# Optimization experiments

Measured on AMD Instinct MI355X. Metric: run time of the kernel, lower is better.

Reference implementation:

```python
import jax, jax.numpy as jnp
import numpy as np

B, L, D, K = 8, 1024, 1024, 128
VOCAB, N_ATOM_FEAT, N_TIMESTEPS = 160, 512, 1000
NEG = jnp.finfo(jnp.float32).min
SCALING = K ** (-0.5)


def setup_inputs() -> dict:
    key = jax.random.key(0)
    ks = jax.random.split(key, 14)
    inp = {}
    # forward args
    inp["token_id"] = jax.random.randint(ks[0], (B, L), 0, VOCAB)  # 0 => padding
    inp["node_attr"] = jax.random.randint(ks[1], (B, L, 9), 0, N_ATOM_FEAT)
    inp["is_molecule"] = jax.random.randint(ks[2], (B,), 0, 2).astype(bool)
    inp["pos"] = jax.random.normal(ks[3], (B, L, 3), jnp.float32) * 10.0
    inp["time_step"] = jax.random.randint(ks[4], (B, L), 0, N_TIMESTEPS)
    # learned parameters
    inp["embed_table"] = jax.random.normal(ks[5], (VOCAB, D), jnp.float32) * 0.02
    inp["atom_feat_table"] = jax.random.normal(ks[6], (N_ATOM_FEAT, D), jnp.float32) * 0.02
    inp["time_table"] = jax.random.normal(ks[7], (N_TIMESTEPS, D), jnp.float32) * 0.02
    inp["time_w1"] = jax.random.normal(ks[8], (D, D), jnp.float32) * (D ** -0.5)
    inp["time_b1"] = jnp.zeros((D,), jnp.float32)
    inp["time_w2"] = jax.random.normal(ks[9], (D, D), jnp.float32) * (D ** -0.5)
    inp["time_b2"] = jnp.zeros((D,), jnp.float32)
    inp["pos_emb_w"] = jax.random.normal(ks[10], (1, K), jnp.float32)          # Linear(1 -> K), no bias
    inp["pos_feature_w"] = jax.random.normal(ks[11], (K, D), jnp.float32) * (K ** -0.5)  # Linear(K -> D), no bias
    return inp


def _pos_emb(pos, padding_mask, pos_emb_w, pos_feature_w):
    # pos: [B,L,3], padding_mask: [B,L] bool
    delta = pos[:, :, None, :] - pos[:, None, :, :]          # [B,L,L,3]
    dist = 1.0 / (jnp.linalg.norm(delta, axis=-1) + 1.0)     # [B,L,L]
    # masked_fill on key side (expand_mask) and query side (padding_mask)
    mask = padding_mask[:, None, :] | padding_mask[:, :, None]
    dist = jnp.where(mask, NEG, dist)
    # value projection: Linear(1->K) on per-atom radial norm, zeroed at padding
    pe = jnp.linalg.norm(pos, axis=-1, keepdims=True) @ pos_emb_w  # [B,L,K]
    pe = jnp.where(padding_mask[:, :, None], 0.0, pe)
    attn = jax.nn.softmax(dist * SCALING, axis=-1)            # [B,L,L]
    pfe = jnp.einsum("bqk,bkc->bqc", attn, pe)                 # [B,L,K]
    pfe = pfe @ pos_feature_w                                  # [B,L,D]
    return jnp.where(padding_mask[:, :, None], 0.0, pfe)


def reference(token_id, node_attr, is_molecule, pos, time_step,
              embed_table, atom_feat_table, time_table,
              time_w1, time_b1, time_w2, time_b2,
              pos_emb_w, pos_feature_w):
    padding_mask = token_id == 0                               # [B,L]
    x = embed_table[token_id]                                  # [B,L,D]
    # 2D atom features: embed cols 1: and sum over feature axis
    atom_emb = atom_feat_table[node_attr[:, :, 1:]].sum(axis=-2)  # [B,L,D]
    atom_emb = jnp.where(is_molecule[:, None, None], atom_emb, 0.0)
    x = x + atom_emb
    # time step encoder: learnable embedding + Linear-SiLU-Linear MLP
    t = time_table[time_step]                                   # [B,L,D]
    time_embed = jax.nn.silu(t @ time_w1 + time_b1) @ time_w2 + time_b2
    x = x + time_embed
    # pairwise 3D positional embedding (softmax attention over 1/(r+1))
    x = x + _pos_emb(pos, padding_mask, pos_emb_w, pos_feature_w)
    return x, padding_mask
```

## Files before the change

kernel.cpp:

```cpp
#include <hip/hip_runtime.h>
#include <hip/hip_bf16.h>
#include <math.h>

#define BB 8
#define LL 1024
#define DD 1024
#define KK 128
#define NTS 1000
#define NEGF -3.40282346638528859811704183485e38f
#define SCALE 0.08838834764831845f

typedef __attribute__((ext_vector_type(8))) short short8;
typedef __attribute__((ext_vector_type(4))) float f32x4;

__device__ __forceinline__ unsigned short f2bf(float x) {
    __hip_bfloat16 h = __float2bfloat16(x);
    return *reinterpret_cast<unsigned short*>(&h);
}

__global__ __launch_bounds__(256) void setup_kernel(
    const float* __restrict__ pos,
    const float* __restrict__ pos_emb_w,
    const float* __restrict__ pos_feature_w,
    const void*  __restrict__ is_mol_raw,
    float* __restrict__ norms,
    float* __restrict__ v,
    int*   __restrict__ is_mol_out)
{
    int gb = blockIdx.x;
    if (gb < 32) {
        int i = gb * 256 + threadIdx.x;
        float x = pos[i * 3 + 0];
        float y = pos[i * 3 + 1];
        float z = pos[i * 3 + 2];
        norms[i] = sqrtf(x * x + y * y + z * z);
    } else if (gb < 36) {
        int d = (gb - 32) * 256 + threadIdx.x;
        float acc = 0.0f;
        #pragma unroll 4
        for (int c = 0; c < KK; ++c)
            acc += pos_emb_w[c] * pos_feature_w[c * DD + d];
        v[d] = acc;
    } else {
        if (threadIdx.x == 0) {
            const int* ip = (const int*)is_mol_raw;
            const unsigned char* cp = (const unsigned char*)is_mol_raw;
            bool all_bin = true;
            for (int i = 0; i < BB; ++i) {
                int x = ip[i];
                if (x != 0 && x != 1) all_bin = false;
            }
            for (int i = 0; i < BB; ++i)
                is_mol_out[i] = all_bin ? (ip[i] != 0) : (cp[i] != 0);
        }
    }
}

__global__ __launch_bounds__(256) void cast_pad_kernel(
    const float* __restrict__ in, unsigned short* __restrict__ out)
{
    int i = blockIdx.x * 256 + threadIdx.x;
    int e = i * 4;
    ushort4 o;
    if (e < NTS * DD) {
        float4 vv = *(const float4*)&in[e];
        o.x = f2bf(vv.x); o.y = f2bf(vv.y); o.z = f2bf(vv.z); o.w = f2bf(vv.w);
    } else {
        o.x = o.y = o.z = o.w = 0;
    }
    *(ushort4*)&out[e] = o;
}

__global__ __launch_bounds__(256) void transpose_cast_kernel(
    const float* __restrict__ in, unsigned short* __restrict__ out)
{
    __shared__ float tile[32][33];
    const int tx = threadIdx.x & 31, ty = threadIdx.x >> 5;
    const int bx = blockIdx.x * 32, by = blockIdx.y * 32;
    #pragma unroll
    for (int r = 0; r < 32; r += 8)
        tile[ty + r][tx] = in[(size_t)(by + ty + r) * DD + bx + tx];
    __syncthreads();
    #pragma unroll
    for (int r = 0; r < 32; r += 8)
        out[(size_t)(bx + ty + r) * DD + by + tx] = f2bf(tile[tx][ty + r]);
}

template <int MODE>
__global__ __launch_bounds__(256) void mfma_gemm(
    const unsigned short* __restrict__ A,
    const unsigned short* __restrict__ Bt,
    const float* __restrict__ bias,
    void* __restrict__ Cout)
{
    __shared__ __align__(16) unsigned short As[64][72];
    __shared__ __align__(16) unsigned short Bs[64][72];

    const int tid  = threadIdx.x;
    const int lane = tid & 63;
    const int wave = tid >> 6;
    const int wm = wave >> 1, wn = wave & 1;
    const int quad = lane >> 4, l16 = lane & 15;
    const int mBase = blockIdx.y * 64, nBase = blockIdx.x * 64;

    f32x4 acc[2][2] = {{{0.f,0.f,0.f,0.f},{0.f,0.f,0.f,0.f}},
                       {{0.f,0.f,0.f,0.f},{0.f,0.f,0.f,0.f}}};

    const int r0 = tid >> 3,           ko0 = (tid & 7) << 3;
    const int r1 = (tid + 256) >> 3,   ko1 = ko0;

    for (int k0 = 0; k0 < DD; k0 += 64) {
        float4 a0 = *(const float4*)&A [(size_t)(mBase + r0) * DD + k0 + ko0];
        float4 a1 = *(const float4*)&A [(size_t)(mBase + r1) * DD + k0 + ko1];
        float4 b0 = *(const float4*)&Bt[(size_t)(nBase + r0) * DD + k0 + ko0];
        float4 b1 = *(const float4*)&Bt[(size_t)(nBase + r1) * DD + k0 + ko1];
        *(float4*)&As[r0][ko0] = a0;
        *(float4*)&As[r1][ko1] = a1;
        *(float4*)&Bs[r0][ko0] = b0;
        *(float4*)&Bs[r1][ko1] = b1;
        __syncthreads();

        #pragma unroll
        for (int kk = 0; kk < 64; kk += 32) {
            short8 af0 = *(const short8*)&As[wm * 32 +      l16][kk + quad * 8];
            short8 af1 = *(const short8*)&As[wm * 32 + 16 + l16][kk + quad * 8];
            short8 bf0 = *(const short8*)&Bs[wn * 32 +      l16][kk + quad * 8];
            short8 bf1 = *(const short8*)&Bs[wn * 32 + 16 + l16][kk + quad * 8];
            acc[0][0] = __builtin_amdgcn_mfma_f32_16x16x32_bf16(af0, bf0, acc[0][0], 0, 0, 0);
            acc[0][1] = __builtin_amdgcn_mfma_f32_16x16x32_bf16(af0, bf1, acc[0][1], 0, 0, 0);
            acc[1][0] = __builtin_amdgcn_mfma_f32_16x16x32_bf16(af1, bf0, acc[1][0], 0, 0, 0);
            acc[1][1] = __builtin_amdgcn_mfma_f32_16x16x32_bf16(af1, bf1, acc[1][1], 0, 0, 0);
        }
        __syncthreads();
    }

    #pragma unroll
    for (int mi = 0; mi < 2; ++mi) {
        #pragma unroll
        for (int ni = 0; ni < 2; ++ni) {
            const int col = nBase + wn * 32 + ni * 16 + l16;
            const float bv = bias[col];
            #pragma unroll
            for (int r = 0; r < 4; ++r) {
                const int row = mBase + wm * 32 + mi * 16 + quad * 4 + r;
                float val = acc[mi][ni][r] + bv;
                if (MODE == 0) {
                    val = val / (1.0f + expf(-val));
                    ((unsigned short*)Cout)[(size_t)row * DD + col] = f2bf(val);
                } else {
                    ((float*)Cout)[(size_t)row * DD + col] = val;
                }
            }
        }
    }
}

__global__ __launch_bounds__(256) void fused_out(
    const int*   __restrict__ token_id,
    const int*   __restrict__ node_attr,
    const float* __restrict__ pos,
    const int*   __restrict__ time_step,
    const float* __restrict__ embed_table,
    const float* __restrict__ atom_feat_table,
    const float* __restrict__ E,
    const float* __restrict__ v,
    const float* __restrict__ norms,
    const int*   __restrict__ is_mol,
    float* __restrict__ out)
{
    __shared__ float redA[256];
    __shared__ float redB[256];

    const int t   = blockIdx.x;
    const int b   = t >> 10;
    const int tid = threadIdx.x;

    const int token = token_id[t];
    const bool padq = (token == 0);

    const float qx = pos[t * 3 + 0];
    const float qy = pos[t * 3 + 1];
    const float qz = pos[t * 3 + 2];

    float dv[4], wv[4];
    float lmax = -INFINITY;
    #pragma unroll
    for (int i = 0; i < 4; ++i) {
        int k = tid + i * 256;
        int kt = token_id[b * LL + k];
        float kx = pos[(b * LL + k) * 3 + 0];
        float ky = pos[(b * LL + k) * 3 + 1];
        float kz = pos[(b * LL + k) * 3 + 2];
        float dx = qx - kx, dy = qy - ky, dz = qz - kz;
        float dn = sqrtf(dx * dx + dy * dy + dz * dz);
        float dist = (padq || kt == 0) ? NEGF : 1.0f / (dn + 1.0f);
        float dsc = dist * SCALE;
        dv[i] = dsc;
        wv[i] = (kt == 0) ? 0.0f : norms[b * LL + k];
        lmax = fmaxf(lmax, dsc);
    }
    redA[tid] = lmax;
    __syncthreads();
    for (int off = 128; off > 0; off >>= 1) {
        if (tid < off) redA[tid] = fmaxf(redA[tid], redA[tid + off]);
        __syncthreads();
    }
    const float gmax = redA[0];
    __syncthreads();

    float lsum = 0.0f, lws = 0.0f;
    #pragma unroll
    for (int i = 0; i < 4; ++i) {
        float e = expf(dv[i] - gmax);
        lsum += e;
        lws  += e * wv[i];
    }
    redA[tid] = lsum;
    redB[tid] = lws;
    __syncthreads();
    for (int off = 128; off > 0; off >>= 1) {
        if (tid < off) {
            redA[tid] += redA[tid + off];
            redB[tid] += redB[tid + off];
        }
        __syncthreads();
    }
    const float s = redB[0] / redA[0];

    const int ts = time_step[t];
    const int j = tid * 4;

    float4 acc = *(const float4*)&embed_table[(size_t)token * DD + j];
    if (is_mol[b]) {
        #pragma unroll
        for (int f = 1; f < 9; ++f) {
            int a = node_attr[t * 9 + f];
            float4 av = *(const float4*)&atom_feat_table[(size_t)a * DD + j];
            acc.x += av.x; acc.y += av.y; acc.z += av.z; acc.w += av.w;
        }
    }
    float4 ev = *(const float4*)&E[(size_t)ts * DD + j];
    acc.x += ev.x; acc.y += ev.y; acc.z += ev.z; acc.w += ev.w;

    if (!padq) {
        float4 vv = *(const float4*)&v[j];
        acc.x += s * vv.x; acc.y += s * vv.y; acc.z += s * vv.z; acc.w += s * vv.w;
    }
    *(float4*)&out[(size_t)t * DD + j] = acc;

    if (tid == 0)
        out[(size_t)BB * LL * DD + t] = padq ? 1.0f : 0.0f;
}

extern "C" void kernel_launch(void* const* d_in, const int* in_sizes, int n_in,
                              void* d_out, int out_size, void* d_ws, size_t ws_size,
                              hipStream_t stream)
{
    const int*   token_id      = (const int*)  d_in[0];
    const int*   node_attr     = (const int*)  d_in[1];
    const void*  is_mol_raw    = (const void*) d_in[2];
    const float* pos           = (const float*)d_in[3];
    const int*   time_step     = (const int*)  d_in[4];
    const float* embed_table   = (const float*)d_in[5];
    const float* atom_feat     = (const float*)d_in[6];
    const float* time_table    = (const float*)d_in[7];
    const float* w1            = (const float*)d_in[8];
    const float* b1            = (const float*)d_in[9];
    const float* w2            = (const float*)d_in[10];
    const float* b2            = (const float*)d_in[11];
    const float* pos_emb_w     = (const float*)d_in[12];
    const float* pos_feature_w = (const float*)d_in[13];

    float* out = (float*)d_out;
    float* Wf  = (float*)d_ws;

    unsigned short* Tbf = (unsigned short*)Wf;
    unsigned short* W1t = (unsigned short*)(Wf + 524288);
    float*          E   = Wf;
    unsigned short* H   = (unsigned short*)(Wf + 1048576);
    unsigned short* W2t = (unsigned short*)(Wf + 1048576 + 524288);
    float* V     = Wf + 2097152;
    float* norms = V + 1024;
    int*   is_mol_res = (int*)(norms + BB * LL);

    setup_kernel<<<37, 256, 0, stream>>>(pos, pos_emb_w, pos_feature_w,
                                         is_mol_raw, norms, V, is_mol_res);
    cast_pad_kernel<<<1024, 256, 0, stream>>>(time_table, Tbf);
    transpose_cast_kernel<<<dim3(32, 32), 256, 0, stream>>>(w1, W1t);
    transpose_cast_kernel<<<dim3(32, 32), 256, 0, stream>>>(w2, W2t);

    dim3 g(16, 16);
    mfma_gemm<0><<<g, 256, 0, stream>>>(Tbf, W1t, b1, (void*)H);
    mfma_gemm<1><<<g, 256, 0, stream>>>(H, W2t, b2, (void*)E);

    fused_out<<<8192, 256, 0, stream>>>(token_id, node_attr, pos, time_step,
                                        embed_table, atom_feat, E, V, norms,
                                        is_mol_res, out);
}
```

Before: 173.1 us.

## Merge prep kernels and restructure softmax to eight queries per block

```diff
diff --git a/kernel.cpp b/kernel.cpp
--- a/kernel.cpp
+++ b/kernel.cpp
@@ -7,7 +7,6 @@
 #define DD 1024
 #define KK 128
 #define NTS 1000
-#define NEGF -3.40282346638528859811704183485e38f
 #define SCALE 0.08838834764831845f
 
 typedef __attribute__((ext_vector_type(8))) short short8;
@@ -18,24 +17,48 @@
     return *reinterpret_cast<unsigned short*>(&h);
 }
 
-__global__ __launch_bounds__(256) void setup_kernel(
-    const float* __restrict__ pos,
+__global__ __launch_bounds__(256) void prep_kernel(
+    const float* __restrict__ time_table,
+    const float* __restrict__ w1,
+    const float* __restrict__ w2,
     const float* __restrict__ pos_emb_w,
     const float* __restrict__ pos_feature_w,
     const void*  __restrict__ is_mol_raw,
-    float* __restrict__ norms,
+    unsigned short* __restrict__ Tbf,
+    unsigned short* __restrict__ W1t,
+    unsigned short* __restrict__ W2t,
     float* __restrict__ v,
     int*   __restrict__ is_mol_out)
 {
-    int gb = blockIdx.x;
-    if (gb < 32) {
-        int i = gb * 256 + threadIdx.x;
-        float x = pos[i * 3 + 0];
-        float y = pos[i * 3 + 1];
-        float z = pos[i * 3 + 2];
-        norms[i] = sqrtf(x * x + y * y + z * z);
-    } else if (gb < 36) {
-        int d = (gb - 32) * 256 + threadIdx.x;
+    __shared__ float tile[32][33];
+    const int blk = blockIdx.x;
+
+    if (blk < 1024) {
+        int e = (blk * 256 + threadIdx.x) * 4;
+        ushort4 o;
+        if (e < NTS * DD) {
+            float4 vv = *(const float4*)&time_table[e];
+            o.x = f2bf(vv.x); o.y = f2bf(vv.y); o.z = f2bf(vv.z); o.w = f2bf(vv.w);
+        } else {
+            o.x = o.y = o.z = o.w = 0;
+        }
+        *(ushort4*)&Tbf[e] = o;
+    } else if (blk < 3072) {
+        const int which = (blk - 1024) >> 10;
+        const int idx = (blk - 1024) & 1023;
+        const float* in = which ? w2 : w1;
+        unsigned short* out = which ? W2t : W1t;
+        const int bx = (idx & 31) * 32, by = (idx >> 5) * 32;
+        const int tx = threadIdx.x & 31, ty = threadIdx.x >> 5;
+        #pragma unroll
+        for (int r = 0; r < 32; r += 8)
+            tile[ty + r][tx] = in[(size_t)(by + ty + r) * DD + bx + tx];
+        __syncthreads();
+        #pragma unroll
+        for (int r = 0; r < 32; r += 8)
+            out[(size_t)(bx + ty + r) * DD + by + tx] = f2bf(tile[tx][ty + r]);
+    } else if (blk < 3076) {
+        int d = (blk - 3072) * 256 + threadIdx.x;
         float acc = 0.0f;
         #pragma unroll 4
         for (int c = 0; c < KK; ++c)
@@ -56,36 +79,6 @@
     }
 }
 
-__global__ __launch_bounds__(256) void cast_pad_kernel(
-    const float* __restrict__ in, unsigned short* __restrict__ out)
-{
-    int i = blockIdx.x * 256 + threadIdx.x;
-    int e = i * 4;
-    ushort4 o;
-    if (e < NTS * DD) {
-        float4 vv = *(const float4*)&in[e];
-        o.x = f2bf(vv.x); o.y = f2bf(vv.y); o.z = f2bf(vv.z); o.w = f2bf(vv.w);
-    } else {
-        o.x = o.y = o.z = o.w = 0;
-    }
-    *(ushort4*)&out[e] = o;
-}
-
-__global__ __launch_bounds__(256) void transpose_cast_kernel(
-    const float* __restrict__ in, unsigned short* __restrict__ out)
-{
-    __shared__ float tile[32][33];
-    const int tx = threadIdx.x & 31, ty = threadIdx.x >> 5;
-    const int bx = blockIdx.x * 32, by = blockIdx.y * 32;
-    #pragma unroll
-    for (int r = 0; r < 32; r += 8)
-        tile[ty + r][tx] = in[(size_t)(by + ty + r) * DD + bx + tx];
-    __syncthreads();
-    #pragma unroll
-    for (int r = 0; r < 32; r += 8)
-        out[(size_t)(bx + ty + r) * DD + by + tx] = f2bf(tile[tx][ty + r]);
-}
-
 template <int MODE>
 __global__ __launch_bounds__(256) void mfma_gemm(
     const unsigned short* __restrict__ A,
@@ -106,8 +99,8 @@
     f32x4 acc[2][2] = {{{0.f,0.f,0.f,0.f},{0.f,0.f,0.f,0.f}},
                        {{0.f,0.f,0.f,0.f},{0.f,0.f,0.f,0.f}}};
 
-    const int r0 = tid >> 3,           ko0 = (tid & 7) << 3;
-    const int r1 = (tid + 256) >> 3,   ko1 = ko0;
+    const int r0 = tid >> 3,         ko0 = (tid & 7) << 3;
+    const int r1 = (tid + 256) >> 3, ko1 = ko0;
 
     for (int k0 = 0; k0 < DD; k0 += 64) {
         float4 a0 = *(const float4*)&A [(size_t)(mBase + r0) * DD + k0 + ko0];
@@ -155,7 +148,7 @@
     }
 }
 
-__global__ __launch_bounds__(256) void fused_out(
+__global__ __launch_bounds__(256) void fused_all(
     const int*   __restrict__ token_id,
     const int*   __restrict__ node_attr,
     const float* __restrict__ pos,
@@ -164,92 +157,88 @@
     const float* __restrict__ atom_feat_table,
     const float* __restrict__ E,
     const float* __restrict__ v,
-    const float* __restrict__ norms,
     const int*   __restrict__ is_mol,
     float* __restrict__ out)
 {
-    __shared__ float redA[256];
-    __shared__ float redB[256];
-
-    const int t   = blockIdx.x;
-    const int b   = t >> 10;
-    const int tid = threadIdx.x;
-
-    const int token = token_id[t];
-    const bool padq = (token == 0);
-
-    const float qx = pos[t * 3 + 0];
-    const float qy = pos[t * 3 + 1];
-    const float qz = pos[t * 3 + 2];
-
-    float dv[4], wv[4];
-    float lmax = -INFINITY;
+    __shared__ float4 keys[LL];
+    __shared__ float  sS[8];
+
+    const int blk   = blockIdx.x;
+    const int batch = blk >> 7;
+    const int q0    = (blk & 127) << 3;
+    const int tid   = threadIdx.x;
+    const int lane  = tid & 63, wave = tid >> 6;
+
     #pragma unroll
     for (int i = 0; i < 4; ++i) {
-        int k = tid + i * 256;
-        int kt = token_id[b * LL + k];
-        float kx = pos[(b * LL + k) * 3 + 0];
-        float ky = pos[(b * LL + k) * 3 + 1];
-        float kz = pos[(b * LL + k) * 3 + 2];
-        float dx = qx - kx, dy = qy - ky, dz = qz - kz;
-        float dn = sqrtf(dx * dx + dy * dy + dz * dz);
-        float dist = (padq || kt == 0) ? NEGF : 1.0f / (dn + 1.0f);
-        float dsc = dist * SCALE;
-        dv[i] = dsc;
-        wv[i] = (kt == 0) ? 0.0f : norms[b * LL + k];
-        lmax = fmaxf(lmax, dsc);
-    }
-    redA[tid] = lmax;
+        const int k = tid + i * 256;
+        const int t = batch * LL + k;
+        const float x = pos[t * 3 + 0];
+        const float y = pos[t * 3 + 1];
+        const float z = pos[t * 3 + 2];
+        const int tok = token_id[t];
+        const float n = sqrtf(x * x + y * y + z * z);
+        keys[k] = make_float4(x, y, z, tok == 0 ? -1.0f : n);
+    }
     __syncthreads();
-    for (int off = 128; off > 0; off >>= 1) {
-        if (tid < off) redA[tid] = fmaxf(redA[tid], redA[tid + off]);
-        __syncthreads();
-    }
-    const float gmax = redA[0];
+
+    #pragma unroll
+    for (int qi = 0; qi < 2; ++qi) {
+        const int ql = wave * 2 + qi;
+        const float4 qk = keys[q0 + ql];
+        float lsum = 0.0f, lws = 0.0f;
+        #pragma unroll 4
+        for (int i = 0; i < 16; ++i) {
+            const float4 kd = keys[lane + i * 64];
+            const float dx = qk.x - kd.x, dy = qk.y - kd.y, dz = qk.z - kd.z;
+            const float dn = sqrtf(dx * dx + dy * dy + dz * dz);
+            const float e = __expf(SCALE / (dn + 1.0f));
+            const bool valid = kd.w >= 0.0f;
+            const float ev = valid ? e : 0.0f;
+            lsum += ev;
+            lws  += ev * (valid ? kd.w : 0.0f);
+        }
+        #pragma unroll
+        for (int off = 32; off > 0; off >>= 1) {
+            lsum += __shfl_xor(lsum, off);
+            lws  += __shfl_xor(lws,  off);
+        }
+        if (lane == 0)
+            sS[ql] = (qk.w < 0.0f) ? 0.0f : (lws / lsum);
+    }
     __syncthreads();
 
-    float lsum = 0.0f, lws = 0.0f;
-    #pragma unroll
-    for (int i = 0; i < 4; ++i) {
-        float e = expf(dv[i] - gmax);
-        lsum += e;
-        lws  += e * wv[i];
-    }
-    redA[tid] = lsum;
-    redB[tid] = lws;
-    __syncthreads();
-    for (int off = 128; off > 0; off >>= 1) {
-        if (tid < off) {
-            redA[tid] += redA[tid + off];
-            redB[tid] += redB[tid + off];
-        }
-        __syncthreads();
-    }
-    const float s = redB[0] / redA[0];
-
-    const int ts = time_step[t];
-    const int j = tid * 4;
-
-    float4 acc = *(const float4*)&embed_table[(size_t)token * DD + j];
-    if (is_mol[b]) {
-        #pragma unroll
-        for (int f = 1; f < 9; ++f) {
-            int a = node_attr[t * 9 + f];
-            float4 av = *(const float4*)&atom_feat_table[(size_t)a * DD + j];
-            acc.x += av.x; acc.y += av.y; acc.z += av.z; acc.w += av.w;
-        }
-    }
-    float4 ev = *(const float4*)&E[(size_t)ts * DD + j];
-    acc.x += ev.x; acc.y += ev.y; acc.z += ev.z; acc.w += ev.w;
-
-    if (!padq) {
-        float4 vv = *(const float4*)&v[j];
-        acc.x += s * vv.x; acc.y += s * vv.y; acc.z += s * vv.z; acc.w += s * vv.w;
-    }
-    *(float4*)&out[(size_t)t * DD + j] = acc;
-
-    if (tid == 0)
-        out[(size_t)BB * LL * DD + t] = padq ? 1.0f : 0.0f;
+    const int im = is_mol[batch];
+    const int j  = tid * 4;
+    const float4 vv = *(const float4*)&v[j];
+
+    for (int ql = 0; ql < 8; ++ql) {
+        const int t   = batch * LL + q0 + ql;
+        const int tok = token_id[t];
+        const int ts  = time_step[t];
+        const float s = sS[ql];
+
+        float4 acc = *(const float4*)&embed_table[(size_t)tok * DD + j];
+        if (im) {
+            #pragma unroll
+            for (int f = 1; f < 9; ++f) {
+                const int a = node_attr[t * 9 + f];
+                const float4 av = *(const float4*)&atom_feat_table[(size_t)a * DD + j];
+                acc.x += av.x; acc.y += av.y; acc.z += av.z; acc.w += av.w;
+            }
+        }
+        const float4 ev = *(const float4*)&E[(size_t)ts * DD + j];
+        acc.x += ev.x + s * vv.x;
+        acc.y += ev.y + s * vv.y;
+        acc.z += ev.z + s * vv.z;
+        acc.w += ev.w + s * vv.w;
+        *(float4*)&out[(size_t)t * DD + j] = acc;
+    }
+
+    if (tid < 8) {
+        const int t = batch * LL + q0 + tid;
+        out[(size_t)BB * LL * DD + t] = (keys[q0 + tid].w < 0.0f) ? 1.0f : 0.0f;
+    }
 }
 
 extern "C" void kernel_launch(void* const* d_in, const int* in_sizes, int n_in,
@@ -280,20 +269,17 @@
     unsigned short* H   = (unsigned short*)(Wf + 1048576);
     unsigned short* W2t = (unsigned short*)(Wf + 1048576 + 524288);
     float* V     = Wf + 2097152;
-    float* norms = V + 1024;
-    int*   is_mol_res = (int*)(norms + BB * LL);
-
-    setup_kernel<<<37, 256, 0, stream>>>(pos, pos_emb_w, pos_feature_w,
-                                         is_mol_raw, norms, V, is_mol_res);
-    cast_pad_kernel<<<1024, 256, 0, stream>>>(time_table, Tbf);
-    transpose_cast_kernel<<<dim3(32, 32), 256, 0, stream>>>(w1, W1t);
-    transpose_cast_kernel<<<dim3(32, 32), 256, 0, stream>>>(w2, W2t);
+    int*   is_mol_res = (int*)(V + 1024);
+
+    prep_kernel<<<3077, 256, 0, stream>>>(time_table, w1, w2, pos_emb_w,
+                                          pos_feature_w, is_mol_raw,
+                                          Tbf, W1t, W2t, V, is_mol_res);
 
     dim3 g(16, 16);
     mfma_gemm<0><<<g, 256, 0, stream>>>(Tbf, W1t, b1, (void*)H);
     mfma_gemm<1><<<g, 256, 0, stream>>>(H, W2t, b2, (void*)E);
 
-    fused_out<<<8192, 256, 0, stream>>>(token_id, node_attr, pos, time_step,
-                                        embed_table, atom_feat, E, V, norms,
+    fused_all<<<1024, 256, 0, stream>>>(token_id, node_attr, pos, time_step,
+                                        embed_table, atom_feat, E, V,
                                         is_mol_res, out);
 }
```

Measured after the change: 158.6 us. 8.3% less time.
